# Optimization experiments

Hardware: AMD Instinct MI355X
Metric: run time of the kernel (lower is better)

Reference implementation:

```python
import jax, jax.numpy as jnp
import numpy as np
import math

T, B, E, H = 1024, 4, 512, 8
HD = E // H

def setup_inputs() -> dict:
    key = jax.random.key(0)
    ks = jax.random.split(key, 6)
    return {
        "query": jax.random.normal(ks[0], (T, B, E), dtype=jnp.float32),
        "dist": jax.random.normal(ks[1], (B, T, T, H), dtype=jnp.float32) * 0.1,
        "in_proj_weight": jax.random.normal(ks[2], (3 * E, E), dtype=jnp.float32) * 0.02,
        "in_proj_bias": jax.random.normal(ks[3], (3 * E,), dtype=jnp.float32) * 0.02,
        "out_proj_weight": jax.random.normal(ks[4], (E, E), dtype=jnp.float32) * 0.02,
        "out_proj_bias": jax.random.normal(ks[5], (E,), dtype=jnp.float32) * 0.02,
    }

def reference(query, dist, in_proj_weight, in_proj_bias, out_proj_weight, out_proj_bias):
    t, b, e = query.shape
    # packed in-projection (self-attention: q=k=v=query)
    qkv = query @ in_proj_weight.T + in_proj_bias          # [T,B,3E]
    q, k, v = jnp.split(qkv, 3, axis=-1)                   # each [T,B,E]
    def heads(x):
        return x.reshape(t, b * H, HD).transpose(1, 0, 2)  # [B*H,T,HD]
    q, k, v = heads(q), heads(k), heads(v)
    q = q / math.sqrt(HD)
    attn = jnp.einsum('bte,bse->bts', q, k)                # [B*H,T,T]
    # distance/structure bias: [B,T,T,H] -> [B,H,T,T] -> [B*H,T,T]
    bias = jnp.transpose(dist, (0, 3, 1, 2)).reshape(b * H, t, t)
    attn = jax.nn.softmax(attn + bias, axis=-1)
    out = jnp.einsum('bts,bse->bte', attn, v)              # [B*H,T,HD]
    out = out.transpose(1, 0, 2).reshape(t, b, e)          # [T,B,E]
    out = out @ out_proj_weight.T + out_proj_bias
    return out
```

## Files before the change

kernel.cpp:

```cpp
#include <hip/hip_runtime.h>
#include <math.h>

typedef __bf16 bf16;
typedef bf16 bf16x8 __attribute__((ext_vector_type(8)));
typedef bf16 bf16x4 __attribute__((ext_vector_type(4)));
typedef float f32x4 __attribute__((ext_vector_type(4)));

#define T_DIM 1024
#define B_DIM 4
#define E_DIM 512
#define H_DIM 8
#define HD_DIM 64
#define BH_DIM 32

__device__ __forceinline__ f32x4 mfma16(bf16x8 a, bf16x8 b, f32x4 c) {
    return __builtin_amdgcn_mfma_f32_16x16x32_bf16(a, b, c, 0, 0, 0);
}

__device__ __forceinline__ bf16x4 cvt4(f32x4 v) {
    bf16x4 o;
    o[0] = (bf16)v[0]; o[1] = (bf16)v[1]; o[2] = (bf16)v[2]; o[3] = (bf16)v[3];
    return o;
}

__global__ __launch_bounds__(256)
void gemm_bt(const float* __restrict__ A, const float* __restrict__ Bt,
             const float* __restrict__ bias, int K, int N, int mode,
             float* __restrict__ out, bf16* __restrict__ qb,
             bf16* __restrict__ kb, bf16* __restrict__ vb) {
    __shared__ __align__(16) bf16 As[64 * 72];
    __shared__ __align__(16) bf16 Bs[64 * 72];
    const int tid  = threadIdx.x;
    const int lane = tid & 63;
    const int wave = tid >> 6;
    const int quad = lane >> 4;
    const int l15  = lane & 15;
    const int wm = wave & 1, wn = wave >> 1;
    const int m0 = blockIdx.x * 64, n0 = blockIdx.y * 64;

    f32x4 acc[2][2] = {};

    const int sr = tid >> 2;
    const int sc = (tid & 3) * 16;

    for (int k0 = 0; k0 < K; k0 += 64) {
#pragma unroll
        for (int j = 0; j < 4; j++) {
            f32x4 av = *(const f32x4*)&A[(long)(m0 + sr) * K + k0 + sc + j * 4];
            *(bf16x4*)&As[sr * 72 + sc + j * 4] = cvt4(av);
            f32x4 bv = *(const f32x4*)&Bt[(long)(n0 + sr) * K + k0 + sc + j * 4];
            *(bf16x4*)&Bs[sr * 72 + sc + j * 4] = cvt4(bv);
        }
        __syncthreads();
#pragma unroll
        for (int kk = 0; kk < 64; kk += 32) {
            bf16x8 a0 = *(const bf16x8*)&As[(wm * 32 + l15) * 72 + kk + quad * 8];
            bf16x8 a1 = *(const bf16x8*)&As[(wm * 32 + 16 + l15) * 72 + kk + quad * 8];
            bf16x8 b0 = *(const bf16x8*)&Bs[(wn * 32 + l15) * 72 + kk + quad * 8];
            bf16x8 b1 = *(const bf16x8*)&Bs[(wn * 32 + 16 + l15) * 72 + kk + quad * 8];
            acc[0][0] = mfma16(a0, b0, acc[0][0]);
            acc[0][1] = mfma16(a0, b1, acc[0][1]);
            acc[1][0] = mfma16(a1, b0, acc[1][0]);
            acc[1][1] = mfma16(a1, b1, acc[1][1]);
        }
        __syncthreads();
    }

#pragma unroll
    for (int mb = 0; mb < 2; mb++) {
#pragma unroll
        for (int nb = 0; nb < 2; nb++) {
            int n = n0 + wn * 32 + nb * 16 + l15;
            float bv = bias[n];
#pragma unroll
            for (int r = 0; r < 4; r++) {
                int m = m0 + wm * 32 + mb * 16 + quad * 4 + r;
                float v = acc[mb][nb][r] + bv;
                if (mode == 0) {
                    out[(long)m * N + n] = v;
                } else {
                    int t = m >> 2, b = m & 3;
                    int sec = n >> 9, j = n & 511;
                    int h = j >> 6, hd = j & 63;
                    long idx = ((long)(b * 8 + h) * T_DIM + t) * HD_DIM + hd;
                    if (sec == 0)      qb[idx] = (bf16)(v * 0.125f);
                    else if (sec == 1) kb[idx] = (bf16)v;
                    else               vb[idx] = (bf16)v;
                }
            }
        }
    }
}

__global__ __launch_bounds__(256)
void attn_kernel(const bf16* __restrict__ qb, const bf16* __restrict__ kb,
                 const bf16* __restrict__ vb, const float* __restrict__ dist,
                 float* __restrict__ ctx) {
    __shared__ __align__(16) bf16 Ks[64 * 72];
    __shared__ __align__(16) bf16 Vts[64 * 72];
    __shared__ __align__(16) bf16 Ps[4 * 16 * 72];
    const int tid  = threadIdx.x;
    const int lane = tid & 63;
    const int wave = tid >> 6;
    const int quad = lane >> 4;
    const int l15  = lane & 15;
    const int bid = blockIdx.x;
    const int h   = bid >> 6;
    const int rem = bid & 63;
    const int b   = rem >> 4;
    const int qt  = rem & 15;
    const int bh  = b * 8 + h;
    const int qrow = qt * 64 + wave * 16 + l15;

    bf16x8 qa0 = *(const bf16x8*)&qb[((long)bh * T_DIM + qrow) * HD_DIM + quad * 8];
    bf16x8 qa1 = *(const bf16x8*)&qb[((long)bh * T_DIM + qrow) * HD_DIM + 32 + quad * 8];

    f32x4 oacc[4] = {};
    float mrun[4], lrun[4];
#pragma unroll
    for (int r = 0; r < 4; r++) { mrun[r] = -INFINITY; lrun[r] = 0.f; }

    const int r0 = tid >> 3;
    const int c0 = (tid & 7) * 8;

    for (int st = 0; st < T_DIM; st += 64) {
        *(bf16x8*)&Ks[r0 * 72 + c0] =
            *(const bf16x8*)&kb[((long)bh * T_DIM + st + r0) * HD_DIM + c0];
        *(bf16x8*)&Ks[(r0 + 32) * 72 + c0] =
            *(const bf16x8*)&kb[((long)bh * T_DIM + st + r0 + 32) * HD_DIM + c0];
        {
            bf16x8 v0 = *(const bf16x8*)&vb[((long)bh * T_DIM + st + r0) * HD_DIM + c0];
            bf16x8 v1 = *(const bf16x8*)&vb[((long)bh * T_DIM + st + r0 + 32) * HD_DIM + c0];
#pragma unroll
            for (int j = 0; j < 8; j++) {
                Vts[(c0 + j) * 72 + r0]      = v0[j];
                Vts[(c0 + j) * 72 + r0 + 32] = v1[j];
            }
        }
        __syncthreads();

        f32x4 sacc[4] = {};
#pragma unroll
        for (int kk = 0; kk < 64; kk += 32) {
            bf16x8 a = (kk == 0) ? qa0 : qa1;
#pragma unroll
            for (int nb = 0; nb < 4; nb++) {
                bf16x8 bfr = *(const bf16x8*)&Ks[(nb * 16 + l15) * 72 + kk + quad * 8];
                sacc[nb] = mfma16(a, bfr, sacc[nb]);
            }
        }

        float sv[4][4];
#pragma unroll
        for (int nb = 0; nb < 4; nb++) {
            int s = st + nb * 16 + l15;
#pragma unroll
            for (int r = 0; r < 4; r++) {
                int tq = qt * 64 + wave * 16 + quad * 4 + r;
                float d = dist[(((long)b * T_DIM + tq) * T_DIM + s) * H_DIM + h];
                sv[nb][r] = sacc[nb][r] + d;
            }
        }

#pragma unroll
        for (int r = 0; r < 4; r++) {
            float rm = fmaxf(fmaxf(sv[0][r], sv[1][r]), fmaxf(sv[2][r], sv[3][r]));
#pragma unroll
            for (int msk = 1; msk < 16; msk <<= 1)
                rm = fmaxf(rm, __shfl_xor(rm, msk));
            float mnew  = fmaxf(mrun[r], rm);
            float alpha = __expf(mrun[r] - mnew);
            mrun[r] = mnew;
            float rs = 0.f;
#pragma unroll
            for (int nb = 0; nb < 4; nb++) {
                float p = __expf(sv[nb][r] - mnew);
                sv[nb][r] = p;
                rs += p;
            }
#pragma unroll
            for (int msk = 1; msk < 16; msk <<= 1)
                rs += __shfl_xor(rs, msk);
            lrun[r] = lrun[r] * alpha + rs;
#pragma unroll
            for (int nb = 0; nb < 4; nb++)
                oacc[nb][r] *= alpha;
        }

        bf16* pw = &Ps[wave * 16 * 72];
#pragma unroll
        for (int nb = 0; nb < 4; nb++)
#pragma unroll
            for (int r = 0; r < 4; r++)
                pw[(quad * 4 + r) * 72 + nb * 16 + l15] = (bf16)sv[nb][r];
        __syncthreads();

#pragma unroll
        for (int kk = 0; kk < 64; kk += 32) {
            bf16x8 ap = *(const bf16x8*)&pw[l15 * 72 + kk + quad * 8];
#pragma unroll
            for (int nb = 0; nb < 4; nb++) {
                bf16x8 bv2 = *(const bf16x8*)&Vts[(nb * 16 + l15) * 72 + kk + quad * 8];
                oacc[nb] = mfma16(ap, bv2, oacc[nb]);
            }
        }
        __syncthreads();
    }

#pragma unroll
    for (int nb = 0; nb < 4; nb++) {
#pragma unroll
        for (int r = 0; r < 4; r++) {
            int t  = qt * 64 + wave * 16 + quad * 4 + r;
            int hd = nb * 16 + l15;
            float o = oacc[nb][r] / lrun[r];
            ctx[((long)t * B_DIM + b) * E_DIM + h * HD_DIM + hd] = o;
        }
    }
}

extern "C" void kernel_launch(void* const* d_in, const int* in_sizes, int n_in,
                              void* d_out, int out_size, void* d_ws, size_t ws_size,
                              hipStream_t stream) {
    const float* query = (const float*)d_in[0];
    const float* dist  = (const float*)d_in[1];
    const float* win   = (const float*)d_in[2];
    const float* bin   = (const float*)d_in[3];
    const float* wout  = (const float*)d_in[4];
    const float* bout  = (const float*)d_in[5];
    float* out = (float*)d_out;

    bf16* qb  = (bf16*)d_ws;
    bf16* kb  = qb + (1 << 21);
    bf16* vb  = kb + (1 << 21);
    float* ctx = (float*)(vb + (1 << 21));

    gemm_bt<<<dim3(64, 24), 256, 0, stream>>>(query, win, bin, 512, 1536, 1,
                                              nullptr, qb, kb, vb);
    attn_kernel<<<dim3(512), 256, 0, stream>>>(qb, kb, vb, dist, ctx);
    gemm_bt<<<dim3(64, 8), 256, 0, stream>>>(ctx, wout, bout, 512, 512, 0,
                                             out, nullptr, nullptr, nullptr);
}
```

Before: 315.3 us.

## Prefetch K/V/dist tiles into registers, pre-transpose V, enlarge GEMM tiles

The attention loop now loads the next tile's K, V and dist-bias values into registers while the current tile is being computed. This is meant to hide global-load latency, especially the strided dist gather. The QKV projection writes V already transposed as [bh][hd][t], so the scalar LDS transpose becomes a vectorized store, and two block barriers per iteration are dropped. The GEMM is templated to 128x128 and 128x64 tiles to get more reuse per block. The cost is higher register pressure and fewer GEMM blocks.

```diff
diff --git a/kernel.cpp b/kernel.cpp
--- a/kernel.cpp
+++ b/kernel.cpp
@@ -23,69 +23,87 @@
     return o;
 }
 
+template<int TM, int TN, int MODE>
 __global__ __launch_bounds__(256)
-void gemm_bt(const float* __restrict__ A, const float* __restrict__ Bt,
-             const float* __restrict__ bias, int K, int N, int mode,
-             float* __restrict__ out, bf16* __restrict__ qb,
-             bf16* __restrict__ kb, bf16* __restrict__ vb) {
-    __shared__ __align__(16) bf16 As[64 * 72];
-    __shared__ __align__(16) bf16 Bs[64 * 72];
+void gemm_t(const float* __restrict__ A, const float* __restrict__ Bt,
+            const float* __restrict__ bias, int K, int N,
+            float* __restrict__ out, bf16* __restrict__ qb,
+            bf16* __restrict__ kb, bf16* __restrict__ vb) {
+    constexpr int FM = TM / 32, FN = TN / 32;
+    __shared__ __align__(16) bf16 As[TM * 72];
+    __shared__ __align__(16) bf16 Bs[TN * 72];
     const int tid  = threadIdx.x;
     const int lane = tid & 63;
     const int wave = tid >> 6;
     const int quad = lane >> 4;
     const int l15  = lane & 15;
     const int wm = wave & 1, wn = wave >> 1;
-    const int m0 = blockIdx.x * 64, n0 = blockIdx.y * 64;
-
-    f32x4 acc[2][2] = {};
+    const int m0 = blockIdx.x * TM, n0 = blockIdx.y * TN;
+
+    f32x4 acc[FM][FN] = {};
 
     const int sr = tid >> 2;
     const int sc = (tid & 3) * 16;
 
     for (int k0 = 0; k0 < K; k0 += 64) {
 #pragma unroll
-        for (int j = 0; j < 4; j++) {
-            f32x4 av = *(const f32x4*)&A[(long)(m0 + sr) * K + k0 + sc + j * 4];
-            *(bf16x4*)&As[sr * 72 + sc + j * 4] = cvt4(av);
-            f32x4 bv = *(const f32x4*)&Bt[(long)(n0 + sr) * K + k0 + sc + j * 4];
-            *(bf16x4*)&Bs[sr * 72 + sc + j * 4] = cvt4(bv);
+        for (int p = 0; p < TM / 64; p++) {
+            const float* src = &A[(long)(m0 + p * 64 + sr) * K + k0 + sc];
+#pragma unroll
+            for (int j = 0; j < 4; j++)
+                *(bf16x4*)&As[(p * 64 + sr) * 72 + sc + j * 4] =
+                    cvt4(*(const f32x4*)(src + j * 4));
+        }
+#pragma unroll
+        for (int p = 0; p < TN / 64; p++) {
+            const float* src = &Bt[(long)(n0 + p * 64 + sr) * K + k0 + sc];
+#pragma unroll
+            for (int j = 0; j < 4; j++)
+                *(bf16x4*)&Bs[(p * 64 + sr) * 72 + sc + j * 4] =
+                    cvt4(*(const f32x4*)(src + j * 4));
         }
         __syncthreads();
 #pragma unroll
         for (int kk = 0; kk < 64; kk += 32) {
-            bf16x8 a0 = *(const bf16x8*)&As[(wm * 32 + l15) * 72 + kk + quad * 8];
-            bf16x8 a1 = *(const bf16x8*)&As[(wm * 32 + 16 + l15) * 72 + kk + quad * 8];
-            bf16x8 b0 = *(const bf16x8*)&Bs[(wn * 32 + l15) * 72 + kk + quad * 8];
-            bf16x8 b1 = *(const bf16x8*)&Bs[(wn * 32 + 16 + l15) * 72 + kk + quad * 8];
-            acc[0][0] = mfma16(a0, b0, acc[0][0]);
-            acc[0][1] = mfma16(a0, b1, acc[0][1]);
-            acc[1][0] = mfma16(a1, b0, acc[1][0]);
-            acc[1][1] = mfma16(a1, b1, acc[1][1]);
-        }
-        __syncthreads();
-    }
-
-#pragma unroll
-    for (int mb = 0; mb < 2; mb++) {
-#pragma unroll
-        for (int nb = 0; nb < 2; nb++) {
-            int n = n0 + wn * 32 + nb * 16 + l15;
+            bf16x8 af[FM], bf[FN];
+#pragma unroll
+            for (int mb = 0; mb < FM; mb++)
+                af[mb] = *(const bf16x8*)&As[(wm * (TM / 2) + mb * 16 + l15) * 72 + kk + quad * 8];
+#pragma unroll
+            for (int nb = 0; nb < FN; nb++)
+                bf[nb] = *(const bf16x8*)&Bs[(wn * (TN / 2) + nb * 16 + l15) * 72 + kk + quad * 8];
+#pragma unroll
+            for (int mb = 0; mb < FM; mb++)
+#pragma unroll
+                for (int nb = 0; nb < FN; nb++)
+                    acc[mb][nb] = mfma16(af[mb], bf[nb], acc[mb][nb]);
+        }
+        __syncthreads();
+    }
+
+#pragma unroll
+    for (int mb = 0; mb < FM; mb++) {
+#pragma unroll
+        for (int nb = 0; nb < FN; nb++) {
+            int n = n0 + wn * (TN / 2) + nb * 16 + l15;
             float bv = bias[n];
 #pragma unroll
             for (int r = 0; r < 4; r++) {
-                int m = m0 + wm * 32 + mb * 16 + quad * 4 + r;
+                int m = m0 + wm * (TM / 2) + mb * 16 + quad * 4 + r;
                 float v = acc[mb][nb][r] + bv;
-                if (mode == 0) {
+                if (MODE == 0) {
                     out[(long)m * N + n] = v;
                 } else {
                     int t = m >> 2, b = m & 3;
                     int sec = n >> 9, j = n & 511;
                     int h = j >> 6, hd = j & 63;
-                    long idx = ((long)(b * 8 + h) * T_DIM + t) * HD_DIM + hd;
-                    if (sec == 0)      qb[idx] = (bf16)(v * 0.125f);
-                    else if (sec == 1) kb[idx] = (bf16)v;
-                    else               vb[idx] = (bf16)v;
+                    int bh = b * 8 + h;
+                    if (sec == 0)
+                        qb[((long)bh * T_DIM + t) * HD_DIM + hd] = (bf16)(v * 0.125f);
+                    else if (sec == 1)
+                        kb[((long)bh * T_DIM + t) * HD_DIM + hd] = (bf16)v;
+                    else
+                        vb[((long)bh * HD_DIM + hd) * T_DIM + t] = (bf16)v;
                 }
             }
         }
@@ -123,21 +141,52 @@
     const int r0 = tid >> 3;
     const int c0 = (tid & 7) * 8;
 
+    bf16x8 pk0, pk1, pv0, pv1;
+    float pb[4][4];
+    {
+        const int st = 0;
+        pk0 = *(const bf16x8*)&kb[((long)bh * T_DIM + st + r0) * HD_DIM + c0];
+        pk1 = *(const bf16x8*)&kb[((long)bh * T_DIM + st + r0 + 32) * HD_DIM + c0];
+        pv0 = *(const bf16x8*)&vb[((long)bh * HD_DIM + r0) * T_DIM + st + c0];
+        pv1 = *(const bf16x8*)&vb[((long)bh * HD_DIM + r0 + 32) * T_DIM + st + c0];
+        const int tqb = qt * 64 + wave * 16 + quad * 4;
+#pragma unroll
+        for (int nb = 0; nb < 4; nb++) {
+            int s = st + nb * 16 + l15;
+#pragma unroll
+            for (int r = 0; r < 4; r++)
+                pb[nb][r] = dist[(((long)b * T_DIM + tqb + r) * T_DIM + s) * H_DIM + h];
+        }
+    }
+
     for (int st = 0; st < T_DIM; st += 64) {
-        *(bf16x8*)&Ks[r0 * 72 + c0] =
-            *(const bf16x8*)&kb[((long)bh * T_DIM + st + r0) * HD_DIM + c0];
-        *(bf16x8*)&Ks[(r0 + 32) * 72 + c0] =
-            *(const bf16x8*)&kb[((long)bh * T_DIM + st + r0 + 32) * HD_DIM + c0];
-        {
-            bf16x8 v0 = *(const bf16x8*)&vb[((long)bh * T_DIM + st + r0) * HD_DIM + c0];
-            bf16x8 v1 = *(const bf16x8*)&vb[((long)bh * T_DIM + st + r0 + 32) * HD_DIM + c0];
-#pragma unroll
-            for (int j = 0; j < 8; j++) {
-                Vts[(c0 + j) * 72 + r0]      = v0[j];
-                Vts[(c0 + j) * 72 + r0 + 32] = v1[j];
-            }
-        }
-        __syncthreads();
+        __syncthreads();
+        *(bf16x8*)&Ks[r0 * 72 + c0]        = pk0;
+        *(bf16x8*)&Ks[(r0 + 32) * 72 + c0] = pk1;
+        *(bf16x8*)&Vts[r0 * 72 + c0]        = pv0;
+        *(bf16x8*)&Vts[(r0 + 32) * 72 + c0] = pv1;
+        float cb[4][4];
+#pragma unroll
+        for (int nb = 0; nb < 4; nb++)
+#pragma unroll
+            for (int r = 0; r < 4; r++) cb[nb][r] = pb[nb][r];
+        __syncthreads();
+
+        if (st + 64 < T_DIM) {
+            const int sn = st + 64;
+            const int tqb = qt * 64 + wave * 16 + quad * 4;
+#pragma unroll
+            for (int nb = 0; nb < 4; nb++) {
+                int s = sn + nb * 16 + l15;
+#pragma unroll
+                for (int r = 0; r < 4; r++)
+                    pb[nb][r] = dist[(((long)b * T_DIM + tqb + r) * T_DIM + s) * H_DIM + h];
+            }
+            pk0 = *(const bf16x8*)&kb[((long)bh * T_DIM + sn + r0) * HD_DIM + c0];
+            pk1 = *(const bf16x8*)&kb[((long)bh * T_DIM + sn + r0 + 32) * HD_DIM + c0];
+            pv0 = *(const bf16x8*)&vb[((long)bh * HD_DIM + r0) * T_DIM + sn + c0];
+            pv1 = *(const bf16x8*)&vb[((long)bh * HD_DIM + r0 + 32) * T_DIM + sn + c0];
+        }
 
         f32x4 sacc[4] = {};
 #pragma unroll
@@ -152,15 +201,10 @@
 
         float sv[4][4];
 #pragma unroll
-        for (int nb = 0; nb < 4; nb++) {
-            int s = st + nb * 16 + l15;
-#pragma unroll
-            for (int r = 0; r < 4; r++) {
-                int tq = qt * 64 + wave * 16 + quad * 4 + r;
-                float d = dist[(((long)b * T_DIM + tq) * T_DIM + s) * H_DIM + h];
-                sv[nb][r] = sacc[nb][r] + d;
-            }
-        }
+        for (int nb = 0; nb < 4; nb++)
+#pragma unroll
+            for (int r = 0; r < 4; r++)
+                sv[nb][r] = sacc[nb][r] + cb[nb][r];
 
 #pragma unroll
         for (int r = 0; r < 4; r++) {
@@ -193,7 +237,6 @@
 #pragma unroll
             for (int r = 0; r < 4; r++)
                 pw[(quad * 4 + r) * 72 + nb * 16 + l15] = (bf16)sv[nb][r];
-        __syncthreads();
 
 #pragma unroll
         for (int kk = 0; kk < 64; kk += 32) {
@@ -204,7 +247,6 @@
                 oacc[nb] = mfma16(ap, bv2, oacc[nb]);
             }
         }
-        __syncthreads();
     }
 
 #pragma unroll
@@ -235,9 +277,9 @@
     bf16* vb  = kb + (1 << 21);
     float* ctx = (float*)(vb + (1 << 21));
 
-    gemm_bt<<<dim3(64, 24), 256, 0, stream>>>(query, win, bin, 512, 1536, 1,
-                                              nullptr, qb, kb, vb);
+    gemm_t<128, 128, 1><<<dim3(32, 12), 256, 0, stream>>>(
+        query, win, bin, 512, 1536, nullptr, qb, kb, vb);
     attn_kernel<<<dim3(512), 256, 0, stream>>>(qb, kb, vb, dist, ctx);
-    gemm_bt<<<dim3(64, 8), 256, 0, stream>>>(ctx, wout, bout, 512, 512, 0,
-                                             out, nullptr, nullptr, nullptr);
-}
+    gemm_t<128, 64, 0><<<dim3(32, 8), 256, 0, stream>>>(
+        ctx, wout, bout, 512, 512, out, nullptr, nullptr, nullptr);
+}
```

Result: faster. 304.8 us (-3.3%).
